# Performance work log

Measured on AMD Instinct MI355X. Metric: run time of the kernel, lower is better.

The kernel has to match this reference:

```python
import jax, jax.numpy as jnp
from jax import lax
import numpy as np

EPS = 1e-5

def _bn(x, g, b):
    # training-mode BatchNorm2d: batch stats over (N,H,W), biased variance
    m = jnp.mean(x, axis=(0, 2, 3), keepdims=True)
    v = jnp.var(x, axis=(0, 2, 3), keepdims=True)
    return g[None, :, None, None] * (x - m) * lax.rsqrt(v + EPS) + b[None, :, None, None]

def _conv(x, w, b, stride=1, pad=0):
    y = lax.conv_general_dilated(x, w, (stride, stride), [(pad, pad), (pad, pad)],
                                 dimension_numbers=('NCHW', 'OIHW', 'NCHW'))
    return y + b[None, :, None, None]

def _convT(x, w, b):
    # torch ConvTranspose2d(k=4, s=2, p=1); w: [in, out, 4, 4]
    wf = jnp.flip(w, (2, 3)).transpose(1, 0, 2, 3)  # -> [out, in, 4, 4]
    y = lax.conv_general_dilated(x, wf, (1, 1), [(2, 2), (2, 2)], lhs_dilation=(2, 2),
                                 dimension_numbers=('NCHW', 'OIHW', 'NCHW'))
    return y + b[None, :, None, None]

def setup_inputs() -> dict:
    key = jax.random.key(0)
    ks = jax.random.split(key, 16)
    B, C_IN, HW = 32, 3, 512
    H_ENC, H_LAT, HID, N_EMB = 16, 2, 64, 3  # Encoder/Decoder hidden, VQ hidden/embed_dim, vqvae hidden, codebook size
    r = lambda k, s: jax.random.normal(k, s, jnp.float32) * 0.05
    return {
        'x': jax.random.normal(ks[0], (B, C_IN, HW, HW), jnp.float32),
        'enc_w1': r(ks[1], (H_ENC, C_IN, 4, 4)), 'enc_b1': r(ks[2], (H_ENC,)),
        'enc_g1': jnp.ones((H_ENC,), jnp.float32), 'enc_be1': jnp.zeros((H_ENC,), jnp.float32),
        'enc_w2': r(ks[3], (HID, H_ENC, 4, 4)), 'enc_b2': r(ks[4], (HID,)),
        'enc_g2': jnp.ones((HID,), jnp.float32), 'enc_be2': jnp.zeros((HID,), jnp.float32),
        'preq_w': r(ks[5], (H_LAT, HID, 1, 1)), 'preq_b': r(ks[6], (H_LAT,)),
        'emb': r(ks[7], (N_EMB, H_LAT)),
        'postq_w': r(ks[8], (HID, H_LAT, 1, 1)), 'postq_b': r(ks[9], (HID,)),
        'dec_w1': r(ks[10], (HID, H_ENC, 4, 4)), 'dec_b1': r(ks[11], (H_ENC,)),
        'dec_g1': jnp.ones((H_ENC,), jnp.float32), 'dec_be1': jnp.zeros((H_ENC,), jnp.float32),
        'dec_w2': r(ks[12], (H_ENC, C_IN, 4, 4)), 'dec_b2': r(ks[13], (C_IN,)),
    }

def reference(x, enc_w1, enc_b1, enc_g1, enc_be1, enc_w2, enc_b2, enc_g2, enc_be2,
              preq_w, preq_b, emb, postq_w, postq_b,
              dec_w1, dec_b1, dec_g1, dec_be1, dec_w2, dec_b2):
    # Encoder
    h = jax.nn.relu(_bn(_conv(x, enc_w1, enc_b1, 2, 1), enc_g1, enc_be1))
    h = jax.nn.relu(_bn(_conv(h, enc_w2, enc_b2, 2, 1), enc_g2, enc_be2))
    # VQ latent space
    q = _conv(h, preq_w, preq_b)                       # [B, 2, H/4, W/4]
    Bq, Cq, Hq, Wq = q.shape
    qf = q.transpose(0, 2, 3, 1).reshape(Bq * Hq * Wq, Cq)
    # squared distances (argmin-equivalent to torch.cdist p=2)
    d2 = jnp.sum(qf**2, -1, keepdims=True) + jnp.sum(emb**2, -1)[None, :] - 2.0 * (qf @ emb.T)
    idx = jnp.argmin(d2, axis=-1)
    e = emb[idx]                                       # gather [N, 2]
    commit = jnp.mean((lax.stop_gradient(e) - qf) ** 2)
    codebook = jnp.mean((e - lax.stop_gradient(qf)) ** 2)
    qloss = codebook + 0.2 * commit
    qout = qf + lax.stop_gradient(e - qf)              # straight-through estimator
    qout = qout.reshape(Bq, Hq, Wq, Cq).transpose(0, 3, 1, 2)
    d = _conv(qout, postq_w, postq_b)
    # Decoder
    d = jax.nn.relu(_bn(_convT(d, dec_w1, dec_b1), dec_g1, dec_be1))
    recon = jnp.tanh(_convT(d, dec_w2, dec_b2))
    return recon, qloss
```

## Files before the change

kernel.cpp:

```cpp
#include <hip/hip_runtime.h>
#include <hip/hip_bf16.h>


#define EPSB 1e-5f

__device__ __forceinline__ float wredf(float v){
#pragma unroll
  for (int m = 32; m >= 1; m >>= 1) v += __shfl_xor(v, m, 64);
  return v;
}

__device__ __forceinline__ float fast_tanh(float x){
  float e = __expf(2.f * x);
  return fmaf(-2.f, __builtin_amdgcn_rcpf(e + 1.f), 1.f);
}

__global__ __launch_bounds__(256) void kP(
    const float* __restrict__ w1, const float* __restrict__ w2,
    const float* __restrict__ dw2,
    const float* __restrict__ pqw, const float* __restrict__ pqb,
    const float* __restrict__ emb,
    float* __restrict__ wt1, float* __restrict__ wt2,
    float* __restrict__ wt9, float* __restrict__ misc)
{
  const int b = blockIdx.x, t = threadIdx.x;
  const int s = b*256 + t;
  { int tap = s >> 6, co = s & 63;
    int ci = tap >> 4, ky = (tap >> 2) & 3, kx = tap & 3;
    wt2[s] = w2[((co*16 + ci)*4 + ky)*4 + kx]; }
  if (b == 0){
    for (int s2 = t; s2 < 768; s2 += 256){
      int tap = s2 >> 4, co = s2 & 15;
      int ci = tap >> 4, ky = (tap >> 2) & 3, kx = tap & 3;
      wt1[s2] = w1[((co*3 + ci)*4 + ky)*4 + kx];
      int ky9 = s2 / 192, rem = s2 - ky9*192;
      int ci9 = rem / 12, r12 = rem - ci9*12;
      int kx9 = r12 / 3, co9 = r12 - kx9*3;
      wt9[s2] = dw2[((ci9*3 + co9)*4 + ky9)*4 + kx9];
    }
    if (t < 192){
      int i = t >> 6, ci = t & 63;
      misc[200 + t] = fmaf(pqw[ci*2], emb[i*2],
                      fmaf(pqw[ci*2 + 1], emb[i*2 + 1], pqb[ci]));
    }
    if (t == 255) misc[192] = 0.f;
  }
}

__global__ __launch_bounds__(64) void k6b_tt(
    const float* __restrict__ dw1, float* __restrict__ misc)
{
  const int e = blockIdx.x;
  const int i = e >> 8, rem = e & 255;
  const int kykx = rem >> 4, oc = rem & 15;
  const int ky = kykx >> 2, kx = kykx & 3;
  const int l = threadIdx.x;
  float v = dw1[((l*16 + oc)*4 + ky)*4 + kx] * misc[200 + i*64 + l];
  v = wredf(v);
  if (l == 0) misc[400 + i*260 + rem] = v;
}

__global__ __launch_bounds__(256) void k1_conv1(
    const float* __restrict__ x, const float* __restrict__ wt1,
    float* __restrict__ h1p, float* __restrict__ part1)
{
  __shared__ __align__(16) float xt[3*6*516];
  __shared__ float red[128];
  const int b = blockIdx.x, t = threadIdx.x;
  const int n = b >> 7, yt = b & 127;
  const int oy0 = yt << 1, iy0 = (oy0 << 1) - 1;
  const int rh = t >> 7, l128 = t & 127, c4 = l128 << 2;
#pragma unroll
  for (int rp = 0; rp < 9; rp++){
    int rIdx = (rp << 1) + rh;
    int ci = rIdx / 6, rr = rIdx - ci*6;
    int iy = iy0 + rr;
    bool yok = (unsigned)iy < 512u;
    const float* xr = x + (((size_t)(n*3 + ci)) << 18) + ((size_t)(iy & 511) << 9);
    float* dst = &xt[rIdx*516];
    float4 v = make_float4(0.f, 0.f, 0.f, 0.f);
    if (yok) v = *(const float4*)&xr[c4];
    dst[c4 + 1] = v.x; dst[c4 + 2] = v.y; dst[c4 + 3] = v.z; dst[c4 + 4] = v.w;
    if (l128 == 0){ dst[0] = 0.f; dst[513] = 0.f; }
  }
  __syncthreads();
  const int w = t >> 6, l = t & 63;
  const int oyr = w & 1, xh = w >> 1;
  float acc[2][16];
#pragma unroll
  for (int j = 0; j < 2; j++)
#pragma unroll
    for (int q = 0; q < 16; q++) acc[j][q] = 0.f;

  for (int ci = 0; ci < 3; ci++){
    for (int ky = 0; ky < 4; ky++){
      const float* xrow = &xt[(ci*6 + (oyr << 1) + ky)*516];
      float v[2][4];
#pragma unroll
      for (int j = 0; j < 2; j++){
        int ox = (xh << 7) + (j << 6) + l;
        float2 p0 = *(const float2*)&xrow[2*ox];
        float2 p1 = *(const float2*)&xrow[2*ox + 2];
        v[j][0] = p0.x; v[j][1] = p0.y; v[j][2] = p1.x; v[j][3] = p1.y;
      }
      const float* wb = &wt1[((ci*4 + ky) << 6)];
#pragma unroll
      for (int kx = 0; kx < 4; kx++){
        const float* wp = wb + (kx << 4);
        float wv[16];
#pragma unroll
        for (int q = 0; q < 16; q++) wv[q] = wp[q];
#pragma unroll
        for (int j = 0; j < 2; j++)
#pragma unroll
          for (int q = 0; q < 16; q++) acc[j][q] = fmaf(v[j][kx], wv[q], acc[j][q]);
      }
    }
  }
  float s[16], ss[16];
#pragma unroll
  for (int q = 0; q < 16; q++){ s[q] = 0.f; ss[q] = 0.f; }
  const int xp = l & 1;
#pragma unroll
  for (int j = 0; j < 2; j++){
    int m = (xh << 6) + (j << 5) + (l >> 1);
#pragma unroll
    for (int q = 0; q < 16; q++){
      float vv = acc[j][q];
      h1p[((((size_t)(n*16 + q) << 1) + oyr) << 15) + ((size_t)xp << 14) + (yt << 7) + m] = vv;
      s[q] += vv; ss[q] += vv*vv;
    }
  }
#pragma unroll
  for (int q = 0; q < 16; q++){ s[q] = wredf(s[q]); ss[q] = wredf(ss[q]); }
  if (l == 0){
#pragma unroll
    for (int q = 0; q < 16; q++){ red[w*32 + q] = s[q]; red[w*32 + 16 + q] = ss[q]; }
  }
  __syncthreads();
  if (t < 32) part1[b*32 + t] = red[t] + red[32+t] + red[64+t] + red[96+t];
}

__global__ __launch_bounds__(256) void k_stats(
    const float* __restrict__ part, int nslots, int slotstride, int grouped,
    const float* __restrict__ g, const float* __restrict__ be,
    float* __restrict__ scale, float* __restrict__ shift, float Ninv)
{
  const int c = blockIdx.x, t = threadIdx.x;
  const int off = grouped ? ((c >> 4) << 5) : 0;
  const int ci = grouped ? (c & 15) : c;
  float S = 0.f, SS = 0.f;
  for (int q = t; q < nslots; q += 256){
    const float* pp = &part[(size_t)q * slotstride + off];
    S += pp[ci]; SS += pp[16 + ci];
  }
  S = wredf(S); SS = wredf(SS);
  __shared__ float sb[8];
  if ((t & 63) == 0){ sb[t >> 6] = S; sb[4 + (t >> 6)] = SS; }
  __syncthreads();
  if (t == 0){
    float Sv = sb[0]+sb[1]+sb[2]+sb[3], SSv = sb[4]+sb[5]+sb[6]+sb[7];
    float m = Sv * Ninv;
    float var = SSv * Ninv - m*m;
    float sc = g[c] * rsqrtf(var + EPSB);
    scale[c] = sc;
    shift[c] = be[c] - m * sc;
  }
}

__global__ __launch_bounds__(256) void k3_conv2(
    const float* __restrict__ h1p, const float* __restrict__ wt2,
    const float* __restrict__ misc, float* __restrict__ h2,
    float* __restrict__ part2)
{
  __shared__ float red[128];
  const int b = blockIdx.x, t = threadIdx.x;
  const int n = b >> 6, yt = b & 63;
  const int oy0 = yt << 1;
  const int w = __builtin_amdgcn_readfirstlane(t >> 6);
  const int l = t & 63, oyr = l >> 5, lx = l & 31;
  float acc[4][16];
#pragma unroll
  for (int e = 0; e < 4; e++)
#pragma unroll
    for (int q = 0; q < 16; q++) acc[e][q] = 0.f;

  const int myk[4] = {oy0 + oyr - 1, oy0 + oyr, oy0 + oyr, oy0 + oyr + 1};
  const int ypk[4] = {1, 0, 1, 0};
  const int lxo = lx << 2;

  for (int g = 0; g < 16; g++){
    const float sc = misc[g], sh = misc[16 + g];
    const float* pg = h1p + (((size_t)(n*16 + g)) << 16);
#pragma unroll
    for (int ky = 0; ky < 4; ky++){
      const int m_y = myk[ky];
      const bool rv = (unsigned)m_y < 128u;
      const int myc = m_y & 127;
      const float scv = rv ? sc : 0.f, shv = rv ? sh : 0.f;
      const float* rb = pg + ((size_t)ypk[ky] << 15) + (myc << 7) + lxo;
      float4 R0 = *(const float4*)rb;
      float4 R1 = *(const float4*)(rb + 16384);
      float A0x = fmaxf(fmaf(R0.x, scv, shv), 0.f);
      float A0y = fmaxf(fmaf(R0.y, scv, shv), 0.f);
      float A0z = fmaxf(fmaf(R0.z, scv, shv), 0.f);
      float A0w = fmaxf(fmaf(R0.w, scv, shv), 0.f);
      float A1x = fmaxf(fmaf(R1.x, scv, shv), 0.f);
      float A1y = fmaxf(fmaf(R1.y, scv, shv), 0.f);
      float A1z = fmaxf(fmaf(R1.z, scv, shv), 0.f);
      float A1w = fmaxf(fmaf(R1.w, scv, shv), 0.f);
      float nx0 = __shfl_down(A0x, 1, 64);  if (lx == 31) nx0 = 0.f;
      float pv1 = __shfl_up(A1w, 1, 64);    if (lx == 0)  pv1 = 0.f;
      float act0[4] = {pv1, A1x, A1y, A1z};
      float act1[4] = {A0x, A0y, A0z, A0w};
      float act2[4] = {A1x, A1y, A1z, A1w};
      float act3[4] = {A0y, A0z, A0w, nx0};
      const float* wb = &wt2[(((g << 4) + (ky << 2)) << 6) + (w << 4)];
#pragma unroll
      for (int kx = 0; kx < 4; kx++){
        const float* wp = wb + (kx << 6);
        float wv[16];
#pragma unroll
        for (int q = 0; q < 16; q++) wv[q] = wp[q];
        const float* av = (kx == 0) ? act0 : (kx == 1) ? act1 : (kx == 2) ? act2 : act3;
#pragma unroll
        for (int e = 0; e < 4; e++)
#pragma unroll
          for (int q = 0; q < 16; q++)
            acc[e][q] = fmaf(av[e], wv[q], acc[e][q]);
      }
    }
  }
  const int oy = oy0 + oyr;
  float s[16], ss[16];
#pragma unroll
  for (int q = 0; q < 16; q++){ s[q] = 0.f; ss[q] = 0.f; }
#pragma unroll
  for (int e = 0; e < 4; e++)
#pragma unroll
    for (int q = 0; q < 16; q++){ float v = acc[e][q]; s[q] += v; ss[q] += v*v; }
#pragma unroll
  for (int q = 0; q < 16; q++){
    float4 o = make_float4(acc[0][q], acc[1][q], acc[2][q], acc[3][q]);
    *(float4*)&h2[(((size_t)(n*64) + (w << 4) + q) << 14) + (oy << 7) + (lx << 2)] = o;
  }
#pragma unroll
  for (int q = 0; q < 16; q++){ s[q] = wredf(s[q]); ss[q] = wredf(ss[q]); }
  if (l == 0){
#pragma unroll
    for (int q = 0; q < 16; q++){ red[w*32 + q] = s[q]; red[w*32 + 16 + q] = ss[q]; }
  }
  __syncthreads();
  if (t < 128) part2[b*128 + t] = red[t];
}

__global__ __launch_bounds__(256) void k5_vq(
    const float* __restrict__ h2, const float* __restrict__ misc,
    const float* __restrict__ pw, const float* __restrict__ pb,
    const float* __restrict__ emb, unsigned char* __restrict__ idxb,
    float* __restrict__ qsum)
{
  __shared__ float eb[4];
  const int t = threadIdx.x;
  const int p0 = blockIdx.x*512 + (t << 1);
  const int n = p0 >> 14, pos = p0 & 16383;
  const float* hp = h2 + ((size_t)n << 20) + pos;
  float q0[2], q1[2];
  const float pb0 = pb[0], pb1 = pb[1];
#pragma unroll
  for (int j = 0; j < 2; j++){ q0[j] = pb0; q1[j] = pb1; }
  for (int c = 0; c < 64; c++){
    float2 v = *(const float2*)&hp[(size_t)c << 14];
    float sc = misc[32 + c], sh = misc[96 + c];
    float w0 = pw[c], w1 = pw[64 + c];
    float a0 = fmaxf(fmaf(v.x, sc, sh), 0.f);
    float a1 = fmaxf(fmaf(v.y, sc, sh), 0.f);
    q0[0] = fmaf(a0, w0, q0[0]); q1[0] = fmaf(a0, w1, q1[0]);
    q0[1] = fmaf(a1, w0, q0[1]); q1[1] = fmaf(a1, w1, q1[1]);
  }
  const float e00 = emb[0], e01 = emb[1], e10 = emb[2], e11 = emb[3],
              e20 = emb[4], e21 = emb[5];
  float esum = 0.f;
  unsigned char bi[2];
#pragma unroll
  for (int j = 0; j < 2; j++){
    float dx0 = q0[j]-e00, dy0 = q1[j]-e01;
    float dx1 = q0[j]-e10, dy1 = q1[j]-e11;
    float dx2 = q0[j]-e20, dy2 = q1[j]-e21;
    float d0 = dx0*dx0+dy0*dy0, d1 = dx1*dx1+dy1*dy1, d2 = dx2*dx2+dy2*dy2;
    int bj = 0; float db = d0;
    if (d1 < db){ db = d1; bj = 1; }
    if (d2 < db){ db = d2; bj = 2; }
    bi[j] = (unsigned char)bj; esum += db;
  }
  *(uchar2*)&idxb[p0] = make_uchar2(bi[0], bi[1]);
  float e = wredf(esum);
  if ((t & 63) == 0) eb[t >> 6] = e;
  __syncthreads();
  if (t == 0) atomicAdd(qsum, eb[0]+eb[1]+eb[2]+eb[3]);
}

__device__ __forceinline__ void d1_accum(const unsigned char* __restrict__ ib,
    int iy, int ix, const float* __restrict__ tt, float* __restrict__ d)
{
  const int py = (iy + 1) & 1, px = (ix + 1) & 1;
#pragma unroll
  for (int kyi = 0; kyi < 2; kyi++){
    int ky = py + 2*kyi, jy = (iy + 1 - ky) >> 1;
    if ((unsigned)jy < 128u){
#pragma unroll
      for (int kxi = 0; kxi < 2; kxi++){
        int kx = px + 2*kxi, jx = (ix + 1 - kx) >> 1;
        if ((unsigned)jx < 128u){
          const float4* tb = (const float4*)&tt[(int)ib[(jy << 7) + jx]*260
                                                + (((ky << 2) + kx) << 4)];
          float4 t0 = tb[0], t1 = tb[1], t2 = tb[2], t3 = tb[3];
          d[0]  += t0.x; d[1]  += t0.y; d[2]  += t0.z; d[3]  += t0.w;
          d[4]  += t1.x; d[5]  += t1.y; d[6]  += t1.z; d[7]  += t1.w;
          d[8]  += t2.x; d[9]  += t2.y; d[10] += t2.z; d[11] += t2.w;
          d[12] += t3.x; d[13] += t3.y; d[14] += t3.z; d[15] += t3.w;
        }
      }
    }
  }
}

__global__ __launch_bounds__(256) void k7s(
    const unsigned char* __restrict__ idxb, const float* __restrict__ misc,
    float* __restrict__ partd, float* __restrict__ qout)
{
  __shared__ __align__(16) float tt[780];
  __shared__ float red[128];
  const int b = blockIdx.x, t = threadIdx.x;
  for (int s = t; s < 780; s += 256) tt[s] = misc[400 + s];
  __syncthreads();
  if (b == 0 && t == 0) qout[0] = 1.2f * misc[192] * (1.0f/1048576.0f);
  float s[16], ss[16];
#pragma unroll
  for (int q = 0; q < 16; q++){ s[q] = 0.f; ss[q] = 0.f; }
  for (int k = 0; k < 4; k++){
    int p = (b << 10) + (k << 8) + t;
    int n = p >> 16, rem = p & 65535, iy = rem >> 8, ix = rem & 255;
    const unsigned char* ib = idxb + ((size_t)n << 14);
    float d[16];
#pragma unroll
    for (int q = 0; q < 16; q++) d[q] = 0.f;
    d1_accum(ib, iy, ix, tt, d);
#pragma unroll
    for (int q = 0; q < 16; q++){ s[q] += d[q]; ss[q] += d[q]*d[q]; }
  }
#pragma unroll
  for (int q = 0; q < 16; q++){ s[q] = wredf(s[q]); ss[q] = wredf(ss[q]); }
  const int w = t >> 6, l = t & 63;
  if (l == 0){
#pragma unroll
    for (int q = 0; q < 16; q++){ red[w*32 + q] = s[q]; red[w*32 + 16 + q] = ss[q]; }
  }
  __syncthreads();
  if (t < 32) partd[b*32 + t] = red[t] + red[32+t] + red[64+t] + red[96+t];
}

__global__ __launch_bounds__(256) void k9_dec(
    const unsigned char* __restrict__ idxb, const float* __restrict__ misc,
    const float* __restrict__ wt9, const float* __restrict__ db2,
    float* __restrict__ out)
{
  __shared__ __align__(16) float a[4*16*132];
  __shared__ __align__(16) float tt[780];
  __shared__ float sd[16], shs[16];
  const int b = blockIdx.x, t = threadIdx.x;
  const int n = b >> 8, r8 = b & 255, G = r8 >> 1, xh = r8 & 1;
  const int M0 = xh << 7;
  for (int s = t; s < 780; s += 256) tt[s] = misc[400 + s];
  if (t < 16){ sd[t] = misc[160 + t]; shs[t] = misc[176 + t]; }
  __syncthreads();
  const unsigned char* ib = idxb + ((size_t)n << 14);
#pragma unroll
  for (int pass = 0; pass < 2; pass++){
    int s = t + (pass << 8);
    int iyr = s >> 7, col = s & 127;
    int iy = (G << 1) - 1 + iyr, ix = M0 + col - 1;
    bool inb = ((unsigned)iy < 256u) && ((unsigned)ix < 256u);
    float d[16];
#pragma unroll
    for (int q = 0; q < 16; q++) d[q] = 0.f;
    if (inb) d1_accum(ib, iy, ix, tt, d);
#pragma unroll
    for (int q = 0; q < 16; q++)
      a[(iyr*16 + q)*132 + col] = inb ? fmaxf(fmaf(d[q], sd[q], shs[q]), 0.f) : 0.f;
  }
  if (t < 8){
    int iyr = t >> 1, col = 128 + (t & 1);
    int iy = (G << 1) - 1 + iyr, ix = M0 + col - 1;
    bool inb = ((unsigned)iy < 256u) && ((unsigned)ix < 256u);
    float d[16];
#pragma unroll
    for (int q = 0; q < 16; q++) d[q] = 0.f;
    if (inb) d1_accum(ib, iy, ix, tt, d);
#pragma unroll
    for (int q = 0; q < 16; q++)
      a[(iyr*16 + q)*132 + col] = inb ? fmaxf(fmaf(d[q], sd[q], shs[q]), 0.f) : 0.f;
  }
  __syncthreads();
  const int rowq = t >> 6, u = t & 63;
  const int oy2 = (G << 2) + rowq;
  const int py = (oy2 + 1) & 1;
  float acc[2][2][3];
#pragma unroll
  for (int p2 = 0; p2 < 2; p2++)
#pragma unroll
    for (int e = 0; e < 2; e++)
#pragma unroll
      for (int c = 0; c < 3; c++) acc[p2][e][c] = 0.f;

#pragma unroll
  for (int kyi = 0; kyi < 2; kyi++){
    const int ky = py + (kyi << 1);
    const int iy = (oy2 + 1 - ky) >> 1;
    if ((unsigned)iy < 256u){
      const int iyr = iy - ((G << 1) - 1);
      for (int ci = 0; ci < 16; ci++){
        const float* wp = &wt9[(ky*16 + ci)*12];
        float w[12];
#pragma unroll
        for (int k = 0; k < 12; k++) w[k] = wp[k];
        const float* ar = &a[(iyr*16 + ci)*132];
        float2 c0 = *(const float2*)&ar[2*u];
        float2 c1 = *(const float2*)&ar[2*u + 2];
        float v[4] = {c0.x, c0.y, c1.x, c1.y};
#pragma unroll
        for (int e = 0; e < 2; e++){
          float vmm = v[e], v0m = v[e+1], vp1 = v[e+2];
          acc[1][e][0] = fmaf(vp1, w[0], acc[1][e][0]);
          acc[1][e][1] = fmaf(vp1, w[1], acc[1][e][1]);
          acc[1][e][2] = fmaf(vp1, w[2], acc[1][e][2]);
          acc[0][e][0] = fmaf(v0m, w[3], acc[0][e][0]);
          acc[0][e][1] = fmaf(v0m, w[4], acc[0][e][1]);
          acc[0][e][2] = fmaf(v0m, w[5], acc[0][e][2]);
          acc[1][e][0] = fmaf(v0m, w[6], acc[1][e][0]);
          acc[1][e][1] = fmaf(v0m, w[7], acc[1][e][1]);
          acc[1][e][2] = fmaf(v0m, w[8], acc[1][e][2]);
          acc[0][e][0] = fmaf(vmm, w[9], acc[0][e][0]);
          acc[0][e][1] = fmaf(vmm, w[10], acc[0][e][1]);
          acc[0][e][2] = fmaf(vmm, w[11], acc[0][e][2]);
        }
      }
    }
  }
  const float bb[3] = {db2[0], db2[1], db2[2]};
#pragma unroll
  for (int co = 0; co < 3; co++){
    float4 o = make_float4(fast_tanh(acc[0][0][co] + bb[co]), fast_tanh(acc[1][0][co] + bb[co]),
                           fast_tanh(acc[0][1][co] + bb[co]), fast_tanh(acc[1][1][co] + bb[co]));
    *(float4*)&out[((size_t)(n*3 + co) << 18) + ((size_t)oy2 << 9) + (M0 << 1) + (u << 2)] = o;
  }
}

extern "C" void kernel_launch(void* const* d_in, const int* in_sizes, int n_in,
                              void* d_out, int out_size, void* d_ws, size_t ws_size,
                              hipStream_t stream)
{
  (void)in_sizes; (void)n_in; (void)out_size;
  const float* x       = (const float*)d_in[0];
  const float* enc_w1  = (const float*)d_in[1];
  const float* enc_g1  = (const float*)d_in[3];
  const float* enc_be1 = (const float*)d_in[4];
  const float* enc_w2  = (const float*)d_in[5];
  const float* enc_g2  = (const float*)d_in[7];
  const float* enc_be2 = (const float*)d_in[8];
  const float* preq_w  = (const float*)d_in[9];
  const float* preq_b  = (const float*)d_in[10];
  const float* emb     = (const float*)d_in[11];
  const float* postq_w = (const float*)d_in[12];
  const float* postq_b = (const float*)d_in[13];
  const float* dec_w1  = (const float*)d_in[14];
  const float* dec_g1  = (const float*)d_in[16];
  const float* dec_be1 = (const float*)d_in[17];
  const float* dec_w2  = (const float*)d_in[18];
  const float* dec_b2  = (const float*)d_in[19];
  float* out = (float*)d_out;
  char*  ws  = (char*)d_ws;

  float* h1p = (float*)ws;
  float* h2  = (float*)(ws + 134217728);
  size_t ebase = (ws_size - 4194304) & ~(size_t)255;
  unsigned char* idxb = (unsigned char*)(ws + ebase);
  float* part1 = (float*)(ws + ebase + 524288);
  float* partd = (float*)(ws + ebase + 1048576);
  float* misc  = (float*)(ws + ebase + 1310720);
  float* wt1   = (float*)(ws + ebase + 1318912);
  float* wt2   = (float*)(ws + ebase + 1327104);
  float* wt9   = (float*)(ws + ebase + 1392640);
  float* part2 = out;

  kP<<<64, 256, 0, stream>>>(enc_w1, enc_w2, dec_w2,
                             postq_w, postq_b, emb, wt1, wt2, wt9, misc);
  k6b_tt<<<768, 64, 0, stream>>>(dec_w1, misc);
  k1_conv1<<<4096, 256, 0, stream>>>(x, wt1, h1p, part1);
  k_stats<<<16, 256, 0, stream>>>(part1, 4096, 32, 0, enc_g1, enc_be1,
                                  misc + 0, misc + 16, 1.f/2097152.f);
  k3_conv2<<<2048, 256, 0, stream>>>(h1p, wt2, misc, h2, part2);
  k_stats<<<64, 256, 0, stream>>>(part2, 2048, 128, 1, enc_g2, enc_be2,
                                  misc + 32, misc + 96, 1.f/524288.f);
  k5_vq<<<1024, 256, 0, stream>>>(h2, misc, preq_w, preq_b, emb, idxb, misc + 192);
  k7s<<<2048, 256, 0, stream>>>(idxb, misc, partd, out + 25165824);
  k_stats<<<16, 256, 0, stream>>>(partd, 2048, 32, 0, dec_g1, dec_be1,
                                  misc + 160, misc + 176, 1.f/2097152.f);
  k9_dec<<<8192, 256, 0, stream>>>(idxb, misc, wt9, dec_b2, out);
}
```

Before: 518.7 us.

## Materialize decoder convT1 output in k7s instead of recomputing in k9_dec

The stats kernel k7s now writes the raw first transposed-conv output (16 channels at 256x256 per image) to workspace memory. The final decoder kernel reads it directly from global memory instead of recomputing it from codebook indices via table lookups into shared memory. This trades recomputation, including halo recomputation, for roughly 128 MB of extra global writes plus the matching reads. The shared-memory staging and its barriers in k9_dec are removed, and BN+ReLU is applied on the fly to the loaded values.

```diff
diff --git a/kernel.cpp b/kernel.cpp
--- a/kernel.cpp
+++ b/kernel.cpp
@@ -327,7 +327,7 @@
 
 __global__ __launch_bounds__(256) void k7s(
     const unsigned char* __restrict__ idxb, const float* __restrict__ misc,
-    float* __restrict__ partd, float* __restrict__ qout)
+    float* __restrict__ d1, float* __restrict__ partd, float* __restrict__ qout)
 {
   __shared__ __align__(16) float tt[780];
   __shared__ float red[128];
@@ -346,8 +346,12 @@
 #pragma unroll
     for (int q = 0; q < 16; q++) d[q] = 0.f;
     d1_accum(ib, iy, ix, tt, d);
-#pragma unroll
-    for (int q = 0; q < 16; q++){ s[q] += d[q]; ss[q] += d[q]*d[q]; }
+    size_t base = ((size_t)(n*16) << 16) + (iy << 8) + ix;
+#pragma unroll
+    for (int q = 0; q < 16; q++){
+      d1[base + ((size_t)q << 16)] = d[q];
+      s[q] += d[q]; ss[q] += d[q]*d[q];
+    }
   }
 #pragma unroll
   for (int q = 0; q < 16; q++){ s[q] = wredf(s[q]); ss[q] = wredf(ss[q]); }
@@ -361,50 +365,21 @@
 }
 
 __global__ __launch_bounds__(256) void k9_dec(
-    const unsigned char* __restrict__ idxb, const float* __restrict__ misc,
+    const float* __restrict__ d1, const float* __restrict__ misc,
     const float* __restrict__ wt9, const float* __restrict__ db2,
     float* __restrict__ out)
 {
-  __shared__ __align__(16) float a[4*16*132];
-  __shared__ __align__(16) float tt[780];
-  __shared__ float sd[16], shs[16];
   const int b = blockIdx.x, t = threadIdx.x;
   const int n = b >> 8, r8 = b & 255, G = r8 >> 1, xh = r8 & 1;
   const int M0 = xh << 7;
-  for (int s = t; s < 780; s += 256) tt[s] = misc[400 + s];
-  if (t < 16){ sd[t] = misc[160 + t]; shs[t] = misc[176 + t]; }
-  __syncthreads();
-  const unsigned char* ib = idxb + ((size_t)n << 14);
-#pragma unroll
-  for (int pass = 0; pass < 2; pass++){
-    int s = t + (pass << 8);
-    int iyr = s >> 7, col = s & 127;
-    int iy = (G << 1) - 1 + iyr, ix = M0 + col - 1;
-    bool inb = ((unsigned)iy < 256u) && ((unsigned)ix < 256u);
-    float d[16];
-#pragma unroll
-    for (int q = 0; q < 16; q++) d[q] = 0.f;
-    if (inb) d1_accum(ib, iy, ix, tt, d);
-#pragma unroll
-    for (int q = 0; q < 16; q++)
-      a[(iyr*16 + q)*132 + col] = inb ? fmaxf(fmaf(d[q], sd[q], shs[q]), 0.f) : 0.f;
-  }
-  if (t < 8){
-    int iyr = t >> 1, col = 128 + (t & 1);
-    int iy = (G << 1) - 1 + iyr, ix = M0 + col - 1;
-    bool inb = ((unsigned)iy < 256u) && ((unsigned)ix < 256u);
-    float d[16];
-#pragma unroll
-    for (int q = 0; q < 16; q++) d[q] = 0.f;
-    if (inb) d1_accum(ib, iy, ix, tt, d);
-#pragma unroll
-    for (int q = 0; q < 16; q++)
-      a[(iyr*16 + q)*132 + col] = inb ? fmaxf(fmaf(d[q], sd[q], shs[q]), 0.f) : 0.f;
-  }
-  __syncthreads();
   const int rowq = t >> 6, u = t & 63;
   const int oy2 = (G << 2) + rowq;
   const int py = (oy2 + 1) & 1;
+  const int ixm = M0 + (u << 1);
+  const bool okl = (ixm - 1) >= 0;
+  const bool okr = (ixm + 2) < 256;
+  const int ixl = okl ? (ixm - 1) : 0;
+  const int ixr = okr ? (ixm + 2) : 255;
   float acc[2][2][3];
 #pragma unroll
   for (int p2 = 0; p2 < 2; p2++)
@@ -418,16 +393,21 @@
     const int ky = py + (kyi << 1);
     const int iy = (oy2 + 1 - ky) >> 1;
     if ((unsigned)iy < 256u){
-      const int iyr = iy - ((G << 1) - 1);
+      const float* R = d1 + ((size_t)(n*16) << 16) + (iy << 8);
       for (int ci = 0; ci < 16; ci++){
+        const float sdv = misc[160 + ci], shv = misc[176 + ci];
         const float* wp = &wt9[(ky*16 + ci)*12];
         float w[12];
 #pragma unroll
         for (int k = 0; k < 12; k++) w[k] = wp[k];
-        const float* ar = &a[(iyr*16 + ci)*132];
-        float2 c0 = *(const float2*)&ar[2*u];
-        float2 c1 = *(const float2*)&ar[2*u + 2];
-        float v[4] = {c0.x, c0.y, c1.x, c1.y};
+        const float* Rc = R + ((size_t)ci << 16);
+        float2 m01 = *(const float2*)&Rc[ixm];
+        float rl = Rc[ixl], rr = Rc[ixr];
+        float v0 = okl ? fmaxf(fmaf(rl,    sdv, shv), 0.f) : 0.f;
+        float v1 =       fmaxf(fmaf(m01.x, sdv, shv), 0.f);
+        float v2 =       fmaxf(fmaf(m01.y, sdv, shv), 0.f);
+        float v3 = okr ? fmaxf(fmaf(rr,    sdv, shv), 0.f) : 0.f;
+        float v[4] = {v0, v1, v2, v3};
 #pragma unroll
         for (int e = 0; e < 2; e++){
           float vmm = v[e], v0m = v[e+1], vp1 = v[e+2];
@@ -492,6 +472,7 @@
   float* wt2   = (float*)(ws + ebase + 1327104);
   float* wt9   = (float*)(ws + ebase + 1392640);
   float* part2 = out;
+  float* d1raw = h1p;
 
   kP<<<64, 256, 0, stream>>>(enc_w1, enc_w2, dec_w2,
                              postq_w, postq_b, emb, wt1, wt2, wt9, misc);
@@ -503,8 +484,8 @@
   k_stats<<<64, 256, 0, stream>>>(part2, 2048, 128, 1, enc_g2, enc_be2,
                                   misc + 32, misc + 96, 1.f/524288.f);
   k5_vq<<<1024, 256, 0, stream>>>(h2, misc, preq_w, preq_b, emb, idxb, misc + 192);
-  k7s<<<2048, 256, 0, stream>>>(idxb, misc, partd, out + 25165824);
+  k7s<<<2048, 256, 0, stream>>>(idxb, misc, d1raw, partd, out + 25165824);
   k_stats<<<16, 256, 0, stream>>>(partd, 2048, 32, 0, dec_g1, dec_be1,
                                   misc + 160, misc + 176, 1.f/2097152.f);
-  k9_dec<<<8192, 256, 0, stream>>>(idxb, misc, wt9, dec_b2, out);
-}
+  k9_dec<<<8192, 256, 0, stream>>>(d1raw, misc, wt9, dec_b2, out);
+}
```

New measurement: 794.0 us. 1.53x slower.
